# Kernel optimization log

Measured on AMD Instinct MI355X. Metric: run time of the kernel, lower is better.

The kernel has to match this reference:

```python
import jax, jax.numpy as jnp
import numpy as np

N_EMBD = 1024
HEAD_SIZE = 64
WINDOW = 64
N_GLOBAL = 64
N_RANDOM = 64
B, T = 8, 2048


def setup_inputs() -> dict:
    key = jax.random.key(0)
    kx, kc, kk, kq, kv = jax.random.split(key, 5)
    x = jax.random.normal(kx, (B, T, N_EMBD), dtype=jnp.float32)
    random_cols = jax.random.randint(kc, (T, N_RANDOM), 0, T)
    s = 1.0 / np.sqrt(N_EMBD)
    Wk = jax.random.normal(kk, (HEAD_SIZE, N_EMBD), dtype=jnp.float32) * s
    Wq = jax.random.normal(kq, (HEAD_SIZE, N_EMBD), dtype=jnp.float32) * s
    Wv = jax.random.normal(kv, (HEAD_SIZE, N_EMBD), dtype=jnp.float32) * s
    return {"x": x, "random_cols": random_cols, "Wk": Wk, "Wq": Wq, "Wv": Wv}


def _bigbird_mask(Tlen, random_cols):
    rows = jnp.arange(Tlen)[:, None]
    cols = jnp.arange(Tlen)[None, :]
    causal = rows >= cols
    local = (cols >= rows - WINDOW + 1) & (cols <= rows)
    glob = (rows < N_GLOBAL) | (cols < N_GLOBAL)
    rand = jnp.zeros((Tlen, Tlen), dtype=bool).at[
        jnp.arange(Tlen)[:, None], random_cols].set(True)
    return (local | glob | rand) & causal  # [T, T] bool


def reference(x, random_cols, Wk, Wq, Wv):
    # projections (Linear, no bias): [B,T,C] @ [C,H] -> [B,T,H]
    k = jnp.einsum('btc,hc->bth', x, Wk)
    q = jnp.einsum('btc,hc->bth', x, Wq)
    v = jnp.einsum('btc,hc->bth', x, Wv)
    scale = 1.0 / jnp.sqrt(jnp.asarray(HEAD_SIZE, x.dtype))
    scores = jnp.einsum('bqh,bkh->bqk', q, k) * scale  # [B,T,T]
    mask = _bigbird_mask(x.shape[1], random_cols)
    scores = jnp.where(mask[None, :, :], scores, -jnp.inf)
    weights = jax.nn.softmax(scores, axis=-1)
    out = jnp.einsum('bqk,bkh->bqh', weights, v)  # [B,T,H]
    return out
```

## Files before the change

kernel.cpp:

```cpp
#include <hip/hip_runtime.h>
#include <math.h>

#define T_DIM 2048
#define C_DIM 1024
#define H_DIM 64
#define M_TOTAL 16384
#define NQKV 192

typedef __bf16 bf16x8 __attribute__((ext_vector_type(8)));
typedef float f32x4 __attribute__((ext_vector_type(4)));
typedef float f32x2 __attribute__((ext_vector_type(2)));
typedef unsigned short u16x8 __attribute__((ext_vector_type(8)));

#if __has_builtin(__builtin_amdgcn_fdot2_f32_bf16)
#define HAVE_DOT2 1
typedef __bf16 bf16x2 __attribute__((ext_vector_type(2)));
#else
#define HAVE_DOT2 0
#endif

#if __has_builtin(__builtin_amdgcn_global_load_lds)
#define HAVE_GLL 1
__device__ __forceinline__ void gload_lds16(const unsigned short* g, unsigned short* l) {
    __builtin_amdgcn_global_load_lds(
        (const __attribute__((address_space(1))) unsigned int*)(const void*)g,
        (__attribute__((address_space(3))) unsigned int*)(void*)l,
        16, 0, 0);
}
#else
#define HAVE_GLL 0
#endif

__device__ __forceinline__ unsigned short f2bf(float f) {
    unsigned u = __float_as_uint(f);
    unsigned r = (u + 0x7FFFu + ((u >> 16) & 1u)) >> 16;
    return (unsigned short)r;
}
__device__ __forceinline__ float bf2f(unsigned short u) {
    return __uint_as_float(((unsigned)u) << 16);
}
__device__ __forceinline__ float blo(unsigned u) { return __uint_as_float(u << 16); }
__device__ __forceinline__ float bhi(unsigned u) { return __uint_as_float(u & 0xFFFF0000u); }
__device__ __forceinline__ unsigned pack_bf2(float f0, float f1) {
    unsigned u0 = __float_as_uint(f0) + 0x8000u;
    unsigned u1 = __float_as_uint(f1) + 0x8000u;
    return __builtin_amdgcn_perm(u1, u0, 0x07060302u);
}
__device__ __forceinline__ uint4 cvt8(float4 a, float4 b) {
    return make_uint4(pack_bf2(a.x, a.y), pack_bf2(a.z, a.w),
                      pack_bf2(b.x, b.y), pack_bf2(b.z, b.w));
}

__device__ __forceinline__ float dot8bf(u16x8 a, u16x8 b, float c) {
#if HAVE_DOT2
    bf16x8 av = __builtin_bit_cast(bf16x8, a);
    bf16x8 bv = __builtin_bit_cast(bf16x8, b);
    #pragma unroll
    for (int e = 0; e < 4; ++e) {
        bf16x2 ap = {av[2 * e], av[2 * e + 1]};
        bf16x2 bp = {bv[2 * e], bv[2 * e + 1]};
        c = __builtin_amdgcn_fdot2_f32_bf16(ap, bp, c, false);
    }
#else
    #pragma unroll
    for (int e = 0; e < 8; ++e) c = fmaf(bf2f(a[e]), bf2f(b[e]), c);
#endif
    return c;
}

#if __has_builtin(__builtin_amdgcn_update_dpp)
#define HAVE_DPP 1
template<int CTRL>
__device__ __forceinline__ float dppf(float x) {
    int v = __builtin_amdgcn_update_dpp(0, __builtin_bit_cast(int, x),
                                        CTRL, 0xF, 0xF, true);
    return __builtin_bit_cast(float, v);
}
__device__ __forceinline__ float red8(float p) {
    p += dppf<0xB1>(p);
    p += dppf<0x4E>(p);
    p += dppf<0x141>(p);
    return p;
}
#else
#define HAVE_DPP 0
__device__ __forceinline__ float red8(float p) {
    p += __shfl_xor(p, 1); p += __shfl_xor(p, 2); p += __shfl_xor(p, 4);
    return p;
}
#endif

__global__ __launch_bounds__(256) void wconv_kernel(
    const float* __restrict__ Wk,
    const float* __restrict__ Wq,
    const float* __restrict__ Wv,
    unsigned short* __restrict__ wbf)
{
    int t   = blockIdx.x * 256 + threadIdx.x;
    int g8  = t & 7;
    int kc  = (t >> 3) & 15;
    int row = t >> 7;
    const float* src = (row < 64)  ? Wk + (size_t)row * C_DIM
                     : (row < 128) ? Wq + (size_t)(row - 64) * C_DIM
                                   : Wv + (size_t)(row - 128) * C_DIM;
    int ksrc = kc * 64 + ((g8 * 8) ^ ((row & 7) * 8));
    float4 a = *(const float4*)(src + ksrc);
    float4 b = *(const float4*)(src + ksrc + 4);
    *(uint4*)(wbf + (size_t)row * C_DIM + kc * 64 + g8 * 8) = cvt8(a, b);
}

__global__ __launch_bounds__(256) void compact_kernel(
    const int* __restrict__ rnd,
    int* __restrict__ rjc,
    int* __restrict__ nvalb)
{
    __shared__ unsigned bm_all[4][64];
    const int wv = threadIdx.x >> 6;
    const int ln = threadIdx.x & 63;
    const int i  = blockIdx.x * 4 + wv;
    unsigned* bm = bm_all[wv];

    bm[ln] = 0u;
    int  j2 = rnd[i * 64 + ln];
    bool v2 = (j2 < i - 63) && (j2 >= 64);
    if (v2) {
        unsigned old = atomicOr(&bm[j2 >> 5], 1u << (j2 & 31));
        v2 = ((old >> (j2 & 31)) & 1u) == 0u;
    }
    unsigned long long mbal = __ballot(v2);
    const int nval = __popcll(mbal);
    if (v2) {
        int pos = __popcll(mbal & ((1ull << ln) - 1ull));
        rjc[i * 64 + pos] = j2;
    }
    if (ln >= nval) rjc[i * 64 + ln] = 0;
    if (ln == 0) nvalb[i] = nval;
}

__global__ __launch_bounds__(512) void proj_kernel(
    const float* __restrict__ x,
    const unsigned short* __restrict__ wbf,
    unsigned short* __restrict__ qkv)
{
    __shared__ unsigned short Ab[64 * 64];
    __shared__ unsigned short Bb[192 * 64];

    const int m0 = blockIdx.x * 64;
    const int t  = threadIdx.x;
    const int wv = t >> 6, ln = t & 63;
    const int mfr = ln & 15, kq = ln >> 4;
    const int r0 = (wv & 1) * 32;
    const int c0 = (wv >> 1) * 48;

    const int srow  = t >> 3;
    const int sk8   = (t & 7) * 8;
    const int skoff = sk8 ^ ((srow & 7) * 8);

    const float* gpx = x + (size_t)(m0 + srow) * C_DIM + sk8;
    unsigned short* lpx = &Ab[srow * 64 + skoff];

    const int wrow = wv * 8 + (ln >> 3);
    const unsigned short* wsrc = wbf + (size_t)wrow * C_DIM + (ln & 7) * 8;

    f32x4 acc[2][3] = {};

    float4 ra = *(const float4*)(gpx);
    float4 rb = *(const float4*)(gpx + 4);

    for (int kc = 0; kc < C_DIM; kc += 64) {
        __syncthreads();
        *(uint4*)lpx = cvt8(ra, rb);
#if HAVE_GLL
        #pragma unroll
        for (int s = 0; s < 3; ++s)
            gload_lds16(wsrc + (size_t)s * 64 * C_DIM + kc,
                        &Bb[(s * 64 + wv * 8) * 64]);
#else
        #pragma unroll
        for (int s = 0; s < 3; ++s) {
            uint4 w4 = *(const uint4*)(wsrc + (size_t)s * 64 * C_DIM + kc);
            *(uint4*)&Bb[(s * 64 + wv * 8 + (ln >> 3)) * 64 + (ln & 7) * 8] = w4;
        }
#endif
        if (kc + 64 < C_DIM) {
            ra = *(const float4*)(gpx + kc + 64);
            rb = *(const float4*)(gpx + kc + 68);
        }
        __syncthreads();
        #pragma unroll
        for (int ks = 0; ks < 64; ks += 32) {
            bf16x8 af[2], bf[3];
            #pragma unroll
            for (int a = 0; a < 2; ++a) {
                int row = r0 + a * 16 + mfr;
                af[a] = *(const bf16x8*)&Ab[row * 64 + ((ks + kq * 8) ^ ((row & 7) * 8))];
            }
            #pragma unroll
            for (int b2 = 0; b2 < 3; ++b2) {
                int row = c0 + b2 * 16 + mfr;
                bf[b2] = *(const bf16x8*)&Bb[row * 64 + ((ks + kq * 8) ^ ((row & 7) * 8))];
            }
            #pragma unroll
            for (int a = 0; a < 2; ++a)
                #pragma unroll
                for (int b2 = 0; b2 < 3; ++b2)
                    acc[a][b2] = __builtin_amdgcn_mfma_f32_16x16x32_bf16(
                        af[a], bf[b2], acc[a][b2], 0, 0, 0);
        }
    }

    #pragma unroll
    for (int a = 0; a < 2; ++a)
        #pragma unroll
        for (int b2 = 0; b2 < 3; ++b2)
            #pragma unroll
            for (int r = 0; r < 4; ++r) {
                int row = m0 + r0 + a * 16 + kq * 4 + r;
                int col = c0 + b2 * 16 + mfr;
                qkv[(size_t)row * NQKV + col] = f2bf(acc[a][b2][r]);
            }
}

__global__ __launch_bounds__(256) void attn_kernel(
    const unsigned short* __restrict__ qkv,
    const int*  __restrict__ rjc,
    const int*  __restrict__ nvalb,
    float* __restrict__ out)
{
    const int wv = threadIdx.x >> 6;
    const int ln = threadIdx.x & 63;
    const int b  = blockIdx.x & 7;
    const int i  = ((blockIdx.x >> 3) << 2) + wv;
    const int bi = b * T_DIM + i;

    const int  nval = nvalb[i];
    const int* rji  = rjc + i * 64;

    const int e8 = (ln & 7) * 8;
    const int gg = ln >> 3;
    u16x8 qraw = *(const u16x8*)(qkv + (size_t)bi * NQKV + 64 + e8);
    const unsigned short* kb = qkv + (size_t)b * T_DIM * NQKV;
    const unsigned short* vb = kb + 128;

    float p[24];

    u16x8 kf[16];
    #pragma unroll
    for (int n = 0; n < 16; ++n) {
        int s = n * 8 + gg;
        int j;
        if (s < 64) { j = i - s; j = (j < 0) ? 0 : j; }
        else        { j = s - 64; }
        kf[n] = *(const u16x8*)(kb + (size_t)j * NQKV + e8);
    }
    #pragma unroll
    for (int n = 0; n < 16; ++n)
        p[n] = red8(dot8bf(kf[n], qraw, 0.f));

    if (nval > 0) {
        u16x8 kr[8];
        #pragma unroll
        for (int u = 0; u < 8; ++u)
            kr[u] = *(const u16x8*)(kb + (size_t)rji[u * 8 + gg] * NQKV + e8);
        #pragma unroll
        for (int u = 0; u < 8; ++u)
            p[16 + u] = red8(dot8bf(kr[u], qraw, 0.f));
    } else {
        #pragma unroll
        for (int u = 0; u < 8; ++u) p[16 + u] = 0.f;
    }

    uint4 vf[16];
    #pragma unroll
    for (int n = 0; n < 16; ++n) {
        int s = n * 8 + gg;
        int j;
        if (s < 64) { j = i - s; j = (j < 0) ? 0 : j; }
        else        { j = s - 64; }
        vf[n] = *(const uint4*)(vb + (size_t)j * NQKV + e8);
    }

    #pragma unroll
    for (int idx = 0; idx < 8; ++idx) {
        bool v = (idx * 8 + gg) <= i;
        p[idx] = v ? p[idx] * 0.125f : -1e30f;
    }
    #pragma unroll
    for (int idx = 8; idx < 16; ++idx) {
        bool v = ((idx - 8) * 8 + gg) < (i - 63);
        p[idx] = v ? p[idx] * 0.125f : -1e30f;
    }
    #pragma unroll
    for (int idx = 16; idx < 24; ++idx) {
        bool v = ((idx - 16) * 8 + gg) < nval;
        p[idx] = v ? p[idx] * 0.125f : -1e30f;
    }

    float mx = p[0];
    #pragma unroll
    for (int idx = 1; idx < 24; ++idx) mx = fmaxf(mx, p[idx]);
    mx = fmaxf(mx, __shfl_xor(mx, 8));
    mx = fmaxf(mx, __shfl_xor(mx, 16));
    mx = fmaxf(mx, __shfl_xor(mx, 32));

    float sum = 0.f;
    #pragma unroll
    for (int idx = 0; idx < 24; ++idx) {
        p[idx] = __expf(p[idx] - mx);
        sum += p[idx];
    }
    sum += __shfl_xor(sum, 8);
    sum += __shfl_xor(sum, 16);
    sum += __shfl_xor(sum, 32);

    f32x2 acc2[4] = {};
    #pragma unroll
    for (int n = 0; n < 16; ++n) {
        float w = p[n];
        f32x2 w2 = {w, w};
        f32x2 p0 = {blo(vf[n].x), bhi(vf[n].x)};
        f32x2 p1 = {blo(vf[n].y), bhi(vf[n].y)};
        f32x2 p2 = {blo(vf[n].z), bhi(vf[n].z)};
        f32x2 p3 = {blo(vf[n].w), bhi(vf[n].w)};
        acc2[0] += w2 * p0;
        acc2[1] += w2 * p1;
        acc2[2] += w2 * p2;
        acc2[3] += w2 * p3;
    }

    if (nval > 0) {
        uint4 vr[8];
        #pragma unroll
        for (int u = 0; u < 8; ++u)
            vr[u] = *(const uint4*)(vb + (size_t)rji[u * 8 + gg] * NQKV + e8);
        #pragma unroll
        for (int u = 0; u < 8; ++u) {
            float w = p[16 + u];
            f32x2 w2 = {w, w};
            f32x2 p0 = {blo(vr[u].x), bhi(vr[u].x)};
            f32x2 p1 = {blo(vr[u].y), bhi(vr[u].y)};
            f32x2 p2 = {blo(vr[u].z), bhi(vr[u].z)};
            f32x2 p3 = {blo(vr[u].w), bhi(vr[u].w)};
            acc2[0] += w2 * p0;
            acc2[1] += w2 * p1;
            acc2[2] += w2 * p2;
            acc2[3] += w2 * p3;
        }
    }

    float acc[8] = { acc2[0][0], acc2[0][1], acc2[1][0], acc2[1][1],
                     acc2[2][0], acc2[2][1], acc2[3][0], acc2[3][1] };
    #pragma unroll
    for (int m = 8; m <= 32; m <<= 1)
        #pragma unroll
        for (int e = 0; e < 8; ++e)
            acc[e] += __shfl_xor(acc[e], m);

    if (ln < 8) {
        float inv = 1.f / sum;
        float* op = &out[(size_t)bi * H_DIM + e8];
        *(float4*)op       = make_float4(acc[0]*inv, acc[1]*inv, acc[2]*inv, acc[3]*inv);
        *(float4*)(op + 4) = make_float4(acc[4]*inv, acc[5]*inv, acc[6]*inv, acc[7]*inv);
    }
}

extern "C" void kernel_launch(void* const* d_in, const int* in_sizes, int n_in,
                              void* d_out, int out_size, void* d_ws, size_t ws_size,
                              hipStream_t stream) {
    const float* x   = (const float*)d_in[0];
    const int*   rnd = (const int*)  d_in[1];
    const float* Wk  = (const float*)d_in[2];
    const float* Wq  = (const float*)d_in[3];
    const float* Wv  = (const float*)d_in[4];
    float* out = (float*)d_out;

    unsigned short* qkv = (unsigned short*)d_ws;
    int* rjc   = (int*)((char*)d_ws + 6291456);
    int* nvalb = rjc + T_DIM * 64;
    unsigned short* wbf = (unsigned short*)((char*)d_ws + 6823936);

    wconv_kernel<<<96, 256, 0, stream>>>(Wk, Wq, Wv, wbf);
    compact_kernel<<<T_DIM / 4, 256, 0, stream>>>(rnd, rjc, nvalb);
    proj_kernel<<<M_TOTAL / 64, 512, 0, stream>>>(x, wbf, qkv);
    attn_kernel<<<M_TOTAL / 4, 256, 0, stream>>>(qkv, rjc, nvalb, out);
}
```

Baseline: 150.5 us.

## Stage shared local and global K/V rows in LDS per 8-query block

The attention kernel now processes 8 queries per 512-thread block and cooperatively loads the union of local-window rows (71) and global rows (64) of K and V into shared memory once. Each wave then reads its window and global keys and values from LDS instead of issuing separate global loads, and the per-wave K/V register arrays are split into chunks of four. This aims to remove redundant global/L2 traffic across neighbouring queries, at the cost of a block-wide barrier, about 34KB of LDS per block and larger blocks, which may lower occupancy.

```diff
diff --git a/kernel.cpp b/kernel.cpp
--- a/kernel.cpp
+++ b/kernel.cpp
@@ -221,41 +221,65 @@
             }
 }
 
-__global__ __launch_bounds__(256) void attn_kernel(
+__global__ __launch_bounds__(512) void attn_kernel(
     const unsigned short* __restrict__ qkv,
     const int*  __restrict__ rjc,
     const int*  __restrict__ nvalb,
     float* __restrict__ out)
 {
-    const int wv = threadIdx.x >> 6;
-    const int ln = threadIdx.x & 63;
+    __shared__ unsigned short st[270 * 64];
+
+    const int t  = threadIdx.x;
+    const int wv = t >> 6;
+    const int ln = t & 63;
     const int b  = blockIdx.x & 7;
-    const int i  = ((blockIdx.x >> 3) << 2) + wv;
+    const int qb = blockIdx.x >> 3;
+    const int i0 = qb * 8;
+    const int i  = i0 + wv;
     const int bi = b * T_DIM + i;
+
+    const unsigned short* kb = qkv + (size_t)b * T_DIM * NQKV;
+    const unsigned short* vb = kb + 128;
+
+    {
+        const int l8 = t & 7;
+        #pragma unroll
+        for (int p = 0; p < 5; ++p) {
+            int si = p * 64 + (t >> 3);
+            if (si < 270) {
+                int tp  = (si < 135) ? si : si - 135;
+                int col = (tp < 71) ? max(i0 - 63 + tp, 0) : tp - 71;
+                const unsigned short* src =
+                    ((si < 135) ? kb : vb) + (size_t)col * NQKV + l8 * 8;
+                *(uint4*)&st[si * 64 + l8 * 8] = *(const uint4*)src;
+            }
+        }
+    }
+    __syncthreads();
 
     const int  nval = nvalb[i];
     const int* rji  = rjc + i * 64;
 
     const int e8 = (ln & 7) * 8;
     const int gg = ln >> 3;
+    const int q  = wv;
     u16x8 qraw = *(const u16x8*)(qkv + (size_t)bi * NQKV + 64 + e8);
-    const unsigned short* kb = qkv + (size_t)b * T_DIM * NQKV;
-    const unsigned short* vb = kb + 128;
 
     float p[24];
 
-    u16x8 kf[16];
-    #pragma unroll
-    for (int n = 0; n < 16; ++n) {
-        int s = n * 8 + gg;
-        int j;
-        if (s < 64) { j = i - s; j = (j < 0) ? 0 : j; }
-        else        { j = s - 64; }
-        kf[n] = *(const u16x8*)(kb + (size_t)j * NQKV + e8);
-    }
-    #pragma unroll
-    for (int n = 0; n < 16; ++n)
-        p[n] = red8(dot8bf(kf[n], qraw, 0.f));
+    #pragma unroll
+    for (int n = 0; n < 16; n += 4) {
+        u16x8 kf[4];
+        #pragma unroll
+        for (int u = 0; u < 4; ++u) {
+            int s   = (n + u) * 8 + gg;
+            int idx = (s < 64) ? (q + 63 - s) : (s + 7);
+            kf[u] = *(const u16x8*)&st[idx * 64 + e8];
+        }
+        #pragma unroll
+        for (int u = 0; u < 4; ++u)
+            p[n + u] = red8(dot8bf(kf[u], qraw, 0.f));
+    }
 
     if (nval > 0) {
         u16x8 kr[8];
@@ -268,16 +292,6 @@
     } else {
         #pragma unroll
         for (int u = 0; u < 8; ++u) p[16 + u] = 0.f;
-    }
-
-    uint4 vf[16];
-    #pragma unroll
-    for (int n = 0; n < 16; ++n) {
-        int s = n * 8 + gg;
-        int j;
-        if (s < 64) { j = i - s; j = (j < 0) ? 0 : j; }
-        else        { j = s - 64; }
-        vf[n] = *(const uint4*)(vb + (size_t)j * NQKV + e8);
     }
 
     #pragma unroll
@@ -315,17 +329,27 @@
 
     f32x2 acc2[4] = {};
     #pragma unroll
-    for (int n = 0; n < 16; ++n) {
-        float w = p[n];
-        f32x2 w2 = {w, w};
-        f32x2 p0 = {blo(vf[n].x), bhi(vf[n].x)};
-        f32x2 p1 = {blo(vf[n].y), bhi(vf[n].y)};
-        f32x2 p2 = {blo(vf[n].z), bhi(vf[n].z)};
-        f32x2 p3 = {blo(vf[n].w), bhi(vf[n].w)};
-        acc2[0] += w2 * p0;
-        acc2[1] += w2 * p1;
-        acc2[2] += w2 * p2;
-        acc2[3] += w2 * p3;
+    for (int n = 0; n < 16; n += 4) {
+        uint4 vf[4];
+        #pragma unroll
+        for (int u = 0; u < 4; ++u) {
+            int s   = (n + u) * 8 + gg;
+            int idx = (s < 64) ? (q + 63 - s) : (s + 7);
+            vf[u] = *(const uint4*)&st[(135 + idx) * 64 + e8];
+        }
+        #pragma unroll
+        for (int u = 0; u < 4; ++u) {
+            float w = p[n + u];
+            f32x2 w2 = {w, w};
+            f32x2 p0 = {blo(vf[u].x), bhi(vf[u].x)};
+            f32x2 p1 = {blo(vf[u].y), bhi(vf[u].y)};
+            f32x2 p2 = {blo(vf[u].z), bhi(vf[u].z)};
+            f32x2 p3 = {blo(vf[u].w), bhi(vf[u].w)};
+            acc2[0] += w2 * p0;
+            acc2[1] += w2 * p1;
+            acc2[2] += w2 * p2;
+            acc2[3] += w2 * p3;
+        }
     }
 
     if (nval > 0) {
@@ -382,5 +406,5 @@
     wconv_kernel<<<96, 256, 0, stream>>>(Wk, Wq, Wv, wbf);
     compact_kernel<<<T_DIM / 4, 256, 0, stream>>>(rnd, rjc, nvalb);
     proj_kernel<<<M_TOTAL / 64, 512, 0, stream>>>(x, wbf, qkv);
-    attn_kernel<<<M_TOTAL / 4, 256, 0, stream>>>(qkv, rjc, nvalb, out);
-}
+    attn_kernel<<<M_TOTAL / 8, 512, 0, stream>>>(qkv, rjc, nvalb, out);
+}
```

Measured after the change: 146.0 us. 3.0% less time.
